# Performance work log

Hardware: AMD Instinct MI355X
Metric: run time of the kernel (lower is better)

The kernel has to match this reference:

```python
import jax, jax.numpy as jnp
import numpy as np

EMBED_DIM = 512
NUM_HEADS = 8
HEAD_DIM = EMBED_DIM // NUM_HEADS
EDGE_HIDDEN = 512
B, L = 2, 512


def setup_inputs() -> dict:
    key = jax.random.key(0)
    ks = jax.random.split(key, 16)
    s = 0.02
    inp = {
        "query": jax.random.normal(ks[0], (B, L, EMBED_DIM), jnp.float32),
        "key_in": jax.random.normal(ks[1], (B, L, EMBED_DIM), jnp.float32),
        "value": jax.random.normal(ks[2], (B, L, EMBED_DIM), jnp.float32),
        "edge_representation": jax.random.normal(ks[3], (B, L, L), jnp.float32),
        # projection weights stored as [in, out]: y = x @ W + b
        "Wq": jax.random.normal(ks[4], (EMBED_DIM, EMBED_DIM), jnp.float32) * s,
        "bq": jnp.zeros((EMBED_DIM,), jnp.float32),
        "Wk": jax.random.normal(ks[5], (EMBED_DIM, EMBED_DIM), jnp.float32) * s,
        "bk": jnp.zeros((EMBED_DIM,), jnp.float32),
        "Wv": jax.random.normal(ks[6], (EMBED_DIM, EMBED_DIM), jnp.float32) * s,
        "bv": jnp.zeros((EMBED_DIM,), jnp.float32),
        "Wo": jax.random.normal(ks[7], (EMBED_DIM, EMBED_DIM), jnp.float32) * s,
        "bo": jnp.zeros((EMBED_DIM,), jnp.float32),
        # edge MLP: Linear(1 -> 512) -> ReLU -> Linear(512 -> num_heads)
        "We1": jax.random.normal(ks[8], (1, EDGE_HIDDEN), jnp.float32) * s,
        "be1": jnp.zeros((EDGE_HIDDEN,), jnp.float32),
        "We2": jax.random.normal(ks[9], (EDGE_HIDDEN, NUM_HEADS), jnp.float32) * s,
        "be2": jnp.zeros((NUM_HEADS,), jnp.float32),
    }
    return inp


def reference(query, key_in, value, edge_representation,
              Wq, bq, Wk, bk, Wv, bv, Wo, bo, We1, be1, We2, be2):
    Bc, Lc, _ = query.shape
    # project and split heads: [B, H, L, Dh]
    def split_heads(x):
        return x.reshape(Bc, Lc, NUM_HEADS, HEAD_DIM).transpose(0, 2, 1, 3)
    Q = split_heads(query @ Wq + bq)
    K = split_heads(key_in @ Wk + bk)
    V = split_heads(value @ Wv + bv)
    # edge MLP on scalar edge features: [B, L, L, 1] -> [B, L, L, H]
    e = edge_representation[..., None]
    h = jax.nn.relu(e * We1[0] + be1)          # [B, L, L, 512]
    edge_bias = h @ We2 + be2                   # [B, L, L, H]
    scale = 1.0 / jnp.sqrt(jnp.asarray(HEAD_DIM, query.dtype))
    scores = jnp.einsum("bhqd,bhkd->bhqk", Q, K) * scale
    scores = scores + edge_bias.transpose(0, 3, 1, 2)  # [B, H, L, L]
    attn = jax.nn.softmax(scores, axis=-1)
    out = jnp.einsum("bhqk,bhkd->bhqd", attn, V)
    out = out.transpose(0, 2, 1, 3).reshape(Bc, Lc, EMBED_DIM)
    return out @ Wo + bo
```

## Files before the change

### kernel.cpp

```cpp
#include <hip/hip_runtime.h>
#include <hip/hip_bf16.h>

typedef __attribute__((ext_vector_type(8))) short bf16x8;
typedef __attribute__((ext_vector_type(4))) float f32x4;

#define LOG2E 1.44269504088896340736f

#define QB_OFF 2621440
#define KB_OFF 3145728
#define VT_OFF 3670016
#define AO_OFF 4194304
#define T_B   9437184
#define A_B   (T_B + 4096)
#define C_B   (A_B + 20480)

struct MegaArgs {
  const float *xq, *xk, *xv, *eg;
  const float *wq, *wk, *wv, *wo;
  const float *bq, *bk, *bv, *bo;
  const float *w1, *b1, *we2, *be2;
  float* out;
  unsigned short* wsb;
  float *wsT, *wsA, *wsC;
};

__device__ __forceinline__ unsigned short f2bf(float f) {
  union { __hip_bfloat16 h; unsigned short u; } c;
  c.h = __float2bfloat16(f);
  return c.u;
}

__device__ __forceinline__ uint4 pack8(float4 a, float4 b) {
  union { unsigned short us[8]; uint4 u; } r;
  r.us[0] = f2bf(a.x); r.us[1] = f2bf(a.y); r.us[2] = f2bf(a.z); r.us[3] = f2bf(a.w);
  r.us[4] = f2bf(b.x); r.us[5] = f2bf(b.y); r.us[6] = f2bf(b.z); r.us[7] = f2bf(b.w);
  return r.u;
}

__device__ __forceinline__ bf16x8 pack8v(float4 a, float4 b) {
  union { uint4 u; bf16x8 v; } r;
  r.u = pack8(a, b);
  return r.v;
}

__device__ void prep_block(const MegaArgs& a, char* smem) {
  float* sT   = (float*)smem;
  int*   sIdx = (int*)(smem + 2048);
  float (*sDA)[8] = (float (*)[8])(smem + 4096);
  float (*sDC)[8] = (float (*)[8])(smem + 20480);
  float* sA0 = (float*)(smem + 36864);
  float* sC0 = (float*)(smem + 36896);
  int tid = threadIdx.x, lane = tid & 63, w = tid >> 6;
  float accA[8] = {0,0,0,0,0,0,0,0}, accC[8] = {0,0,0,0,0,0,0,0};
  for (int e = 0; e < 2; ++e) {
    int p = tid + e * 256;
    float ww = a.w1[p], bb = a.b1[p];
    sT[p] = (ww != 0.f) ? (-bb / ww) : -3.4e38f;
    sIdx[p] = p;
#pragma unroll
    for (int h = 0; h < 8; ++h) {
      float w2 = a.we2[p * 8 + h];
      if (ww < 0.f)       { accA[h] += w2 * ww; accC[h] += w2 * bb; }
      else if (ww == 0.f) { accC[h] += w2 * fmaxf(bb, 0.f); }
    }
  }
  __syncthreads();
  for (int size = 2; size <= 512; size <<= 1) {
    for (int stride = size >> 1; stride > 0; stride >>= 1) {
      if (size >= 256 && stride >= 64) __syncthreads();
      else __builtin_amdgcn_wave_barrier();
      int p = tid;
      int i = ((p / stride) * (stride << 1)) + (p % stride);
      int j = i + stride;
      bool up = ((i & size) == 0);
      float ti = sT[i], tj = sT[j];
      if (up ? (ti > tj) : (ti < tj)) {
        sT[i] = tj; sT[j] = ti;
        int t = sIdx[i]; sIdx[i] = sIdx[j]; sIdx[j] = t;
      }
    }
  }
  for (int off = 32; off > 0; off >>= 1) {
#pragma unroll
    for (int h = 0; h < 8; ++h) {
      accA[h] += __shfl_xor(accA[h], off);
      accC[h] += __shfl_xor(accC[h], off);
    }
  }
  if (lane == 0) {
#pragma unroll
    for (int h = 0; h < 8; ++h) { sDA[w][h] = accA[h]; sDC[w][h] = accC[h]; }
  }
  __syncthreads();
  if (tid < 8) {
    sA0[tid] = sDA[0][tid] + sDA[1][tid] + sDA[2][tid] + sDA[3][tid];
    sC0[tid] = sDC[0][tid] + sDC[1][tid] + sDC[2][tid] + sDC[3][tid] + a.be2[tid];
  }
  __syncthreads();
  for (int e = 0; e < 2; ++e) {
    int p = tid + e * 256;
    int k = sIdx[p];
    float wk = a.w1[k], bk2 = a.b1[k];
#pragma unroll
    for (int h = 0; h < 8; ++h) {
      float w2 = a.we2[k * 8 + h];
      float da = 0.f, dc = 0.f;
      if (wk > 0.f)      { da =  w2 * wk; dc =  w2 * bk2; }
      else if (wk < 0.f) { da = -w2 * wk; dc = -w2 * bk2; }
      sDA[p][h] = da; sDC[p][h] = dc;
    }
  }
  __syncthreads();
  for (int off = 1; off < 512; off <<= 1) {
    float ra[2][8], rc[2][8];
#pragma unroll
    for (int e = 0; e < 2; ++e) {
      int p = tid + e * 256;
      if (p >= off) {
#pragma unroll
        for (int h = 0; h < 8; ++h) { ra[e][h] = sDA[p - off][h]; rc[e][h] = sDC[p - off][h]; }
      }
    }
    __syncthreads();
#pragma unroll
    for (int e = 0; e < 2; ++e) {
      int p = tid + e * 256;
      if (p >= off) {
#pragma unroll
        for (int h = 0; h < 8; ++h) { sDA[p][h] += ra[e][h]; sDC[p][h] += rc[e][h]; }
      }
    }
    __syncthreads();
  }
  bool n0 = (tid == 0) || (sT[tid] != sT[tid - 1]);
  bool n1 = (sT[tid + 256] != sT[tid + 255]);
  unsigned long long m0 = __ballot(n0), m1 = __ballot(n1);
  unsigned long long below = (1ull << lane) - 1ull;
  int loc0 = __popcll(m0 & below), loc1 = __popcll(m1 & below);
  int* tot = sIdx;
  if (lane == 0) { tot[w] = __popcll(m0); tot[4 + w] = __popcll(m1); }
  __syncthreads();
  int t[8];
#pragma unroll
  for (int j = 0; j < 8; ++j) t[j] = tot[j];
  int nuniq = t[0] + t[1] + t[2] + t[3] + t[4] + t[5] + t[6] + t[7];
  int off0 = 0, off1 = t[0] + t[1] + t[2] + t[3];
  for (int j = 0; j < 4; ++j) {
    if (j < w) { off0 += t[j]; off1 += t[4 + j]; }
  }
  if (n0) {
    int u = off0 + loc0;
    a.wsT[u] = sT[tid];
    if (tid == 0) {
#pragma unroll
      for (int h = 0; h < 8; ++h) { a.wsA[h * 513] = sA0[h]; a.wsC[h * 513] = sC0[h]; }
    } else {
#pragma unroll
      for (int h = 0; h < 8; ++h) {
        a.wsA[h * 513 + u] = sA0[h] + sDA[tid - 1][h];
        a.wsC[h * 513 + u] = sC0[h] + sDC[tid - 1][h];
      }
    }
  }
  if (n1) {
    int u = off1 + loc1;
    a.wsT[u] = sT[tid + 256];
#pragma unroll
    for (int h = 0; h < 8; ++h) {
      a.wsA[h * 513 + u] = sA0[h] + sDA[tid + 255][h];
      a.wsC[h * 513 + u] = sC0[h] + sDC[tid + 255][h];
    }
  }
  if (tid == 0) {
#pragma unroll
    for (int h = 0; h < 8; ++h) {
      a.wsA[h * 513 + nuniq] = sA0[h] + sDA[511][h];
      a.wsC[h * 513 + nuniq] = sC0[h] + sDC[511][h];
    }
    *(int*)(a.wsT + 512) = nuniq;
  }
}

__device__ void gemm_fast(const float* __restrict__ Af, const unsigned short* __restrict__ Ab,
                          const float* __restrict__ W, const float* __restrict__ bias,
                          void* out, int mode, int m0, int n0, char* smem) {
  int tid = threadIdx.x, wave = tid >> 6, lane = tid & 63;
  int quad = lane >> 4, l16 = lane & 15;
  int lr = tid >> 2, ls = tid & 3;
  int kb8 = lr >> 3, klo = lr & 7;
  int slot = ((kb8 ^ ls) << 3) + klo;
#pragma unroll
  for (int c = 0; c < 8; ++c) {
    unsigned short (*sBt)[72] = (unsigned short (*)[72])(smem + c * 9216);
    const float4* wp = (const float4*)(W + (size_t)(c * 64 + lr) * 512 + n0 + ls * 16);
    float4 w0 = wp[0], w1 = wp[1], w2 = wp[2], w3 = wp[3];
    int nb = ls * 16;
    sBt[nb + 0][slot] = f2bf(w0.x);  sBt[nb + 1][slot] = f2bf(w0.y);
    sBt[nb + 2][slot] = f2bf(w0.z);  sBt[nb + 3][slot] = f2bf(w0.w);
    sBt[nb + 4][slot] = f2bf(w1.x);  sBt[nb + 5][slot] = f2bf(w1.y);
    sBt[nb + 6][slot] = f2bf(w1.z);  sBt[nb + 7][slot] = f2bf(w1.w);
    sBt[nb + 8][slot] = f2bf(w2.x);  sBt[nb + 9][slot] = f2bf(w2.y);
    sBt[nb + 10][slot] = f2bf(w2.z); sBt[nb + 11][slot] = f2bf(w2.w);
    sBt[nb + 12][slot] = f2bf(w3.x); sBt[nb + 13][slot] = f2bf(w3.y);
    sBt[nb + 14][slot] = f2bf(w3.z); sBt[nb + 15][slot] = f2bf(w3.w);
  }
  __syncthreads();
  f32x4 acc[4] = {{0.f,0.f,0.f,0.f},{0.f,0.f,0.f,0.f},{0.f,0.f,0.f,0.f},{0.f,0.f,0.f,0.f}};
  const float*          arf = Af ? Af + (size_t)(m0 + wave * 16 + l16) * 512 : nullptr;
  const unsigned short* arb = Ab ? Ab + (size_t)(m0 + wave * 16 + l16) * 512 : nullptr;
#pragma unroll
  for (int kf = 0; kf < 16; ++kf) {
    bf16x8 af;
    if (Af) {
      const float4* ap = (const float4*)(arf + kf * 32 + quad * 8);
      af = pack8v(ap[0], ap[1]);
    } else {
      af = *(const bf16x8*)(arb + kf * 32 + quad * 8);
    }
    unsigned short (*sBt)[72] = (unsigned short (*)[72])(smem + (kf >> 1) * 9216);
    int g = (kf & 1) * 4 + quad;
#pragma unroll
    for (int nt = 0; nt < 4; ++nt) {
      bf16x8 bf = *(const bf16x8*)&sBt[nt * 16 + l16][(g ^ nt) * 8];
      acc[nt] = __builtin_amdgcn_mfma_f32_16x16x32_bf16(af, bf, acc[nt], 0, 0, 0);
    }
  }
  int mbase = m0 + wave * 16 + quad * 4;
#pragma unroll
  for (int nt = 0; nt < 4; ++nt) {
    int n = n0 + nt * 16 + l16;
    float bv = bias[n];
#pragma unroll
    for (int r = 0; r < 4; ++r) {
      float v = acc[nt][r] + bv;
      int m = mbase + r;
      if (mode == 0) {
        int b = m >> 9, l = m & 511, hh = n >> 6, d = n & 63;
        ((unsigned short*)out)[(((size_t)(b * 8 + hh) * 512) + l) * 64 + d] = f2bf(v);
      } else if (mode == 1) {
        ((float*)out)[(size_t)m * 512 + n] = v;
      } else {
        int b = m >> 9, l = m & 511, hh = n >> 6, d = n & 63;
        ((unsigned short*)out)[(((size_t)(b * 8 + hh) * 64) + d) * 512 + l] = f2bf(v);
      }
    }
  }
}

__device__ void attn_block(const MegaArgs& a, int qt, int h, int b, char* smem) {
  float* sT  = (float*)smem;
  float* sAh = (float*)(smem + 2048);
  float* sCh = (float*)(smem + 4112);
  unsigned short (*sP)[16][136] = (unsigned short (*)[16][136])(smem + 6176);
  float (*sO)[4][16][16] = (float (*)[4][16][16])(smem + 23584);
  float (*sM)[16] = (float (*)[16])(smem + 39968);
  float (*sL)[16] = (float (*)[16])(smem + 40224);
  const unsigned short* Qb = a.wsb + QB_OFF;
  const unsigned short* Kb = a.wsb + KB_OFF;
  const unsigned short* Vt = a.wsb + VT_OFF;
  int bh = b * 8 + h;
  int q0 = qt * 16;
  int tid = threadIdx.x, wave = tid >> 6, lane = tid & 63;
  int quad = lane >> 4, l16 = lane & 15;
  int nu = *(const int*)(a.wsT + 512);
  for (int i = tid; i < nu; i += 256) sT[i] = a.wsT[i];
  for (int i = tid; i <= nu; i += 256) { sAh[i] = a.wsA[h * 513 + i]; sCh[i] = a.wsC[h * 513 + i]; }
  int key_base = wave * 128;
  float egv[4][2][4];
#pragma unroll
  for (int kt = 0; kt < 4; ++kt)
#pragma unroll
    for (int half = 0; half < 2; ++half)
#pragma unroll
      for (int r = 0; r < 4; ++r) {
        int eidx = (b * 512 + q0 + quad * 4 + r) * 512 + key_base + kt * 32 + half * 16 + l16;
        egv[kt][half][r] = a.eg[eidx];
      }
  const unsigned short* qp = Qb + ((size_t)bh * 512 + q0 + l16) * 64 + quad * 8;
  bf16x8 qf0 = *(const bf16x8*)qp;
  bf16x8 qf1 = *(const bf16x8*)(qp + 32);
  bf16x8 kfr[4][2][2];
#pragma unroll
  for (int kt = 0; kt < 4; ++kt)
#pragma unroll
    for (int half = 0; half < 2; ++half) {
      const unsigned short* kp =
          Kb + ((size_t)bh * 512 + key_base + kt * 32 + half * 16 + l16) * 64 + quad * 8;
      kfr[kt][half][0] = *(const bf16x8*)kp;
      kfr[kt][half][1] = *(const bf16x8*)(kp + 32);
    }
  f32x4 S[4][2];
#pragma unroll
  for (int kt = 0; kt < 4; ++kt)
#pragma unroll
    for (int half = 0; half < 2; ++half) {
      f32x4 acc = {0.f, 0.f, 0.f, 0.f};
      acc = __builtin_amdgcn_mfma_f32_16x16x32_bf16(qf0, kfr[kt][half][0], acc, 0, 0, 0);
      acc = __builtin_amdgcn_mfma_f32_16x16x32_bf16(qf1, kfr[kt][half][1], acc, 0, 0, 0);
      S[kt][half] = acc;
    }
  __syncthreads();
#pragma unroll
  for (int kt = 0; kt < 4; ++kt)
#pragma unroll
    for (int half = 0; half < 2; ++half)
#pragma unroll
      for (int r = 0; r < 4; ++r) {
        float ev = egv[kt][half][r];
        int lo = 0, hi = nu;
        while (lo < hi) {
          int mid = (lo + hi) >> 1;
          bool c = sT[mid] < ev;
          lo = c ? mid + 1 : lo;
          hi = c ? hi : mid;
        }
        S[kt][half][r] = S[kt][half][r] * 0.125f + sAh[lo] * ev + sCh[lo];
      }
  bf16x8 vfr[4][4];
#pragma unroll
  for (int kt = 0; kt < 4; ++kt)
#pragma unroll
    for (int nt = 0; nt < 4; ++nt)
      vfr[kt][nt] = *(const bf16x8*)(Vt + ((size_t)bh * 64 + nt * 16 + l16) * 512 +
                                     key_base + kt * 32 + quad * 8);
  float m_w[4], l_w[4];
#pragma unroll
  for (int r = 0; r < 4; ++r) {
    float mx = -3.4e38f;
#pragma unroll
    for (int kt = 0; kt < 4; ++kt) { mx = fmaxf(mx, fmaxf(S[kt][0][r], S[kt][1][r])); }
    for (int off = 1; off < 16; off <<= 1) mx = fmaxf(mx, __shfl_xor(mx, off, 64));
    float s = 0.f;
#pragma unroll
    for (int kt = 0; kt < 4; ++kt)
#pragma unroll
      for (int half = 0; half < 2; ++half) {
        float p = exp2f((S[kt][half][r] - mx) * LOG2E);
        S[kt][half][r] = p; s += p;
      }
    for (int off = 1; off < 16; off <<= 1) s += __shfl_xor(s, off, 64);
    m_w[r] = mx; l_w[r] = s;
  }
#pragma unroll
  for (int kt = 0; kt < 4; ++kt)
#pragma unroll
    for (int half = 0; half < 2; ++half)
#pragma unroll
      for (int r = 0; r < 4; ++r)
        sP[wave][quad * 4 + r][kt * 32 + half * 16 + l16] = f2bf(S[kt][half][r]);
  __builtin_amdgcn_wave_barrier();
  f32x4 Oacc[4] = {{0.f,0.f,0.f,0.f},{0.f,0.f,0.f,0.f},{0.f,0.f,0.f,0.f},{0.f,0.f,0.f,0.f}};
#pragma unroll
  for (int kt = 0; kt < 4; ++kt) {
    bf16x8 pf = *(const bf16x8*)&sP[wave][l16][kt * 32 + quad * 8];
#pragma unroll
    for (int nt = 0; nt < 4; ++nt)
      Oacc[nt] = __builtin_amdgcn_mfma_f32_16x16x32_bf16(pf, vfr[kt][nt], Oacc[nt], 0, 0, 0);
  }
  if (l16 == 0) {
#pragma unroll
    for (int r = 0; r < 4; ++r) { sM[wave][quad * 4 + r] = m_w[r]; sL[wave][quad * 4 + r] = l_w[r]; }
  }
#pragma unroll
  for (int nt = 0; nt < 4; ++nt)
#pragma unroll
    for (int r = 0; r < 4; ++r)
      sO[wave][nt][quad * 4 + r][l16] = Oacc[nt][r];
  __syncthreads();
#pragma unroll
  for (int r = 0; r < 4; ++r) {
    int row = quad * 4 + r;
    float M = fmaxf(fmaxf(sM[0][row], sM[1][row]), fmaxf(sM[2][row], sM[3][row]));
    float L = 0.f, Ov = 0.f;
#pragma unroll
    for (int wv = 0; wv < 4; ++wv) {
      float f = exp2f((sM[wv][row] - M) * LOG2E);
      L += f * sL[wv][row];
      Ov += f * sO[wv][wave][row][l16];
    }
    float v = Ov / L;
    (a.wsb + AO_OFF)[((size_t)(b * 512 + q0 + row)) * 512 + h * 64 + wave * 16 + l16] = f2bf(v);
  }
}

__global__ __launch_bounds__(256, 2) void k1(MegaArgs a) {
  __shared__ __align__(16) char smem[73728];
  int blk = blockIdx.x;
  if (blk == 0) {
    prep_block(a, smem);
  } else {
    int g = blk - 1, z = g >> 7, rem = g & 127;
    const float* A    = (z == 0) ? a.xq : (z == 1) ? a.xk : a.xv;
    const float* W    = (z == 0) ? a.wq : (z == 1) ? a.wk : a.wv;
    const float* bias = (z == 0) ? a.bq : (z == 1) ? a.bk : a.bv;
    void* outp = (void*)(a.wsb + ((z == 0) ? QB_OFF : (z == 1) ? KB_OFF : VT_OFF));
    gemm_fast(A, nullptr, W, bias, outp, (z == 2) ? 2 : 0, (rem & 15) * 64, (rem >> 4) * 64, smem);
  }
}

__global__ __launch_bounds__(256, 2) void k2(MegaArgs a) {
  __shared__ __align__(16) char smem[40480];
  int blk = blockIdx.x;
  attn_block(a, blk & 31, (blk >> 5) & 7, blk >> 8, smem);
}

__global__ __launch_bounds__(256, 2) void k3(MegaArgs a) {
  __shared__ __align__(16) char smem[73728];
  gemm_fast(nullptr, a.wsb + AO_OFF, a.wo, a.bo, (void*)a.out, 1,
            (blockIdx.x & 15) * 64, (blockIdx.x >> 4) * 64, smem);
}

extern "C" void kernel_launch(void* const* d_in, const int* in_sizes, int n_in,
                              void* d_out, int out_size, void* d_ws, size_t ws_size,
                              hipStream_t stream) {
  MegaArgs a;
  a.xq  = (const float*)d_in[0];
  a.xk  = (const float*)d_in[1];
  a.xv  = (const float*)d_in[2];
  a.eg  = (const float*)d_in[3];
  a.wq  = (const float*)d_in[4];
  a.bq  = (const float*)d_in[5];
  a.wk  = (const float*)d_in[6];
  a.bk  = (const float*)d_in[7];
  a.wv  = (const float*)d_in[8];
  a.bv  = (const float*)d_in[9];
  a.wo  = (const float*)d_in[10];
  a.bo  = (const float*)d_in[11];
  a.w1  = (const float*)d_in[12];
  a.b1  = (const float*)d_in[13];
  a.we2 = (const float*)d_in[14];
  a.be2 = (const float*)d_in[15];
  a.out = (float*)d_out;
  a.wsb = (unsigned short*)d_ws;
  a.wsT = (float*)((char*)d_ws + T_B);
  a.wsA = (float*)((char*)d_ws + A_B);
  a.wsC = (float*)((char*)d_ws + C_B);

  k1<<<385, 256, 0, stream>>>(a);
  k2<<<512, 256, 0, stream>>>(a);
  k3<<<128, 256, 0, stream>>>(a);
}
```

Measured before the change: 134.9 us.

## Fuse three kernels into one persistent kernel with global atomic barriers

Merges the projection, attention and output-projection kernels into a single 512-block launch separated by software grid barriers built on agent-scope atomics, with a memset resetting the counters each call. The edge-MLP prep block signals readiness through a separate flag, so attention blocks can run their QK^T MFMAs before waiting on it. K and V fragments are now loaded next to their MFMAs instead of being preloaded into register arrays. The aim is to remove kernel launch gaps and hide the prep latency. In exchange it depends on all 512 blocks being co-resident, since the grid barrier deadlocks otherwise, and it adds spin-wait and memset overhead.

```diff
diff --git a/kernel.cpp b/kernel.cpp
--- a/kernel.cpp
+++ b/kernel.cpp
@@ -13,6 +13,8 @@
 #define T_B   9437184
 #define A_B   (T_B + 4096)
 #define C_B   (A_B + 20480)
+#define BAR_B 16777216
+#define NBLK  512
 
 struct MegaArgs {
   const float *xq, *xk, *xv, *eg;
@@ -41,6 +43,20 @@
   union { uint4 u; bf16x8 v; } r;
   r.u = pack8(a, b);
   return r.v;
+}
+
+__device__ __forceinline__ void gbar(unsigned int* cnt, unsigned int target, int arrive) {
+  __syncthreads();
+  if (threadIdx.x == 0) {
+    __threadfence();
+    if (arrive)
+      __hip_atomic_fetch_add(cnt, 1u, __ATOMIC_RELEASE, __HIP_MEMORY_SCOPE_AGENT);
+    while (__hip_atomic_load(cnt, __ATOMIC_ACQUIRE, __HIP_MEMORY_SCOPE_AGENT) < target) {
+      __builtin_amdgcn_s_sleep(8);
+    }
+    __threadfence();
+  }
+  __syncthreads();
 }
 
 __device__ void prep_block(const MegaArgs& a, char* smem) {
@@ -247,7 +263,8 @@
   }
 }
 
-__device__ void attn_block(const MegaArgs& a, int qt, int h, int b, char* smem) {
+__device__ void attn_block6(const MegaArgs& a, int qt, int h, int b, char* smem,
+                            unsigned int* flag) {
   float* sT  = (float*)smem;
   float* sAh = (float*)(smem + 2048);
   float* sCh = (float*)(smem + 4112);
@@ -262,43 +279,45 @@
   int q0 = qt * 16;
   int tid = threadIdx.x, wave = tid >> 6, lane = tid & 63;
   int quad = lane >> 4, l16 = lane & 15;
+  int key_base = wave * 128;
+  float egv[4][2][4];
+#pragma unroll
+  for (int kt = 0; kt < 4; ++kt)
+#pragma unroll
+    for (int half = 0; half < 2; ++half)
+#pragma unroll
+      for (int r = 0; r < 4; ++r) {
+        int eidx = (b * 512 + q0 + quad * 4 + r) * 512 + key_base + kt * 32 + half * 16 + l16;
+        egv[kt][half][r] = a.eg[eidx];
+      }
+  const unsigned short* qp = Qb + ((size_t)bh * 512 + q0 + l16) * 64 + quad * 8;
+  bf16x8 qf0 = *(const bf16x8*)qp;
+  bf16x8 qf1 = *(const bf16x8*)(qp + 32);
+  f32x4 S[4][2];
+#pragma unroll
+  for (int kt = 0; kt < 4; ++kt) {
+    int key0 = key_base + kt * 32;
+#pragma unroll
+    for (int half = 0; half < 2; ++half) {
+      const unsigned short* kp = Kb + ((size_t)bh * 512 + key0 + half * 16 + l16) * 64 + quad * 8;
+      bf16x8 kf0 = *(const bf16x8*)kp;
+      bf16x8 kf1 = *(const bf16x8*)(kp + 32);
+      f32x4 acc = {0.f, 0.f, 0.f, 0.f};
+      acc = __builtin_amdgcn_mfma_f32_16x16x32_bf16(qf0, kf0, acc, 0, 0, 0);
+      acc = __builtin_amdgcn_mfma_f32_16x16x32_bf16(qf1, kf1, acc, 0, 0, 0);
+      S[kt][half] = acc;
+    }
+  }
+  if (tid == 0) {
+    while (__hip_atomic_load(flag, __ATOMIC_ACQUIRE, __HIP_MEMORY_SCOPE_AGENT) == 0u) {
+      __builtin_amdgcn_s_sleep(8);
+    }
+    __threadfence();
+  }
+  __syncthreads();
   int nu = *(const int*)(a.wsT + 512);
   for (int i = tid; i < nu; i += 256) sT[i] = a.wsT[i];
   for (int i = tid; i <= nu; i += 256) { sAh[i] = a.wsA[h * 513 + i]; sCh[i] = a.wsC[h * 513 + i]; }
-  int key_base = wave * 128;
-  float egv[4][2][4];
-#pragma unroll
-  for (int kt = 0; kt < 4; ++kt)
-#pragma unroll
-    for (int half = 0; half < 2; ++half)
-#pragma unroll
-      for (int r = 0; r < 4; ++r) {
-        int eidx = (b * 512 + q0 + quad * 4 + r) * 512 + key_base + kt * 32 + half * 16 + l16;
-        egv[kt][half][r] = a.eg[eidx];
-      }
-  const unsigned short* qp = Qb + ((size_t)bh * 512 + q0 + l16) * 64 + quad * 8;
-  bf16x8 qf0 = *(const bf16x8*)qp;
-  bf16x8 qf1 = *(const bf16x8*)(qp + 32);
-  bf16x8 kfr[4][2][2];
-#pragma unroll
-  for (int kt = 0; kt < 4; ++kt)
-#pragma unroll
-    for (int half = 0; half < 2; ++half) {
-      const unsigned short* kp =
-          Kb + ((size_t)bh * 512 + key_base + kt * 32 + half * 16 + l16) * 64 + quad * 8;
-      kfr[kt][half][0] = *(const bf16x8*)kp;
-      kfr[kt][half][1] = *(const bf16x8*)(kp + 32);
-    }
-  f32x4 S[4][2];
-#pragma unroll
-  for (int kt = 0; kt < 4; ++kt)
-#pragma unroll
-    for (int half = 0; half < 2; ++half) {
-      f32x4 acc = {0.f, 0.f, 0.f, 0.f};
-      acc = __builtin_amdgcn_mfma_f32_16x16x32_bf16(qf0, kfr[kt][half][0], acc, 0, 0, 0);
-      acc = __builtin_amdgcn_mfma_f32_16x16x32_bf16(qf1, kfr[kt][half][1], acc, 0, 0, 0);
-      S[kt][half] = acc;
-    }
   __syncthreads();
 #pragma unroll
   for (int kt = 0; kt < 4; ++kt)
@@ -316,13 +335,6 @@
         }
         S[kt][half][r] = S[kt][half][r] * 0.125f + sAh[lo] * ev + sCh[lo];
       }
-  bf16x8 vfr[4][4];
-#pragma unroll
-  for (int kt = 0; kt < 4; ++kt)
-#pragma unroll
-    for (int nt = 0; nt < 4; ++nt)
-      vfr[kt][nt] = *(const bf16x8*)(Vt + ((size_t)bh * 64 + nt * 16 + l16) * 512 +
-                                     key_base + kt * 32 + quad * 8);
   float m_w[4], l_w[4];
 #pragma unroll
   for (int r = 0; r < 4; ++r) {
@@ -352,10 +364,13 @@
   f32x4 Oacc[4] = {{0.f,0.f,0.f,0.f},{0.f,0.f,0.f,0.f},{0.f,0.f,0.f,0.f},{0.f,0.f,0.f,0.f}};
 #pragma unroll
   for (int kt = 0; kt < 4; ++kt) {
+    int key0 = key_base + kt * 32;
     bf16x8 pf = *(const bf16x8*)&sP[wave][l16][kt * 32 + quad * 8];
 #pragma unroll
-    for (int nt = 0; nt < 4; ++nt)
-      Oacc[nt] = __builtin_amdgcn_mfma_f32_16x16x32_bf16(pf, vfr[kt][nt], Oacc[nt], 0, 0, 0);
+    for (int nt = 0; nt < 4; ++nt) {
+      bf16x8 vf = *(const bf16x8*)(Vt + ((size_t)bh * 64 + nt * 16 + l16) * 512 + key0 + quad * 8);
+      Oacc[nt] = __builtin_amdgcn_mfma_f32_16x16x32_bf16(pf, vf, Oacc[nt], 0, 0, 0);
+    }
   }
   if (l16 == 0) {
 #pragma unroll
@@ -383,31 +398,42 @@
   }
 }
 
-__global__ __launch_bounds__(256, 2) void k1(MegaArgs a) {
+__global__ __launch_bounds__(256, 2) void kfused(MegaArgs a) {
   __shared__ __align__(16) char smem[73728];
+  unsigned int* bar0 = (unsigned int*)((char*)a.wsb + BAR_B);
+  unsigned int* flag = bar0 + 16;
+  unsigned int* bar1 = bar0 + 32;
   int blk = blockIdx.x;
+
   if (blk == 0) {
     prep_block(a, smem);
+    __syncthreads();
+    if (threadIdx.x == 0) {
+      __threadfence();
+      __hip_atomic_store(flag, 1u, __ATOMIC_RELEASE, __HIP_MEMORY_SCOPE_AGENT);
+    }
+    gbar(bar0, NBLK - 1, 0);
   } else {
-    int g = blk - 1, z = g >> 7, rem = g & 127;
-    const float* A    = (z == 0) ? a.xq : (z == 1) ? a.xk : a.xv;
-    const float* W    = (z == 0) ? a.wq : (z == 1) ? a.wk : a.wv;
-    const float* bias = (z == 0) ? a.bq : (z == 1) ? a.bk : a.bv;
-    void* outp = (void*)(a.wsb + ((z == 0) ? QB_OFF : (z == 1) ? KB_OFF : VT_OFF));
-    gemm_fast(A, nullptr, W, bias, outp, (z == 2) ? 2 : 0, (rem & 15) * 64, (rem >> 4) * 64, smem);
-  }
-}
-
-__global__ __launch_bounds__(256, 2) void k2(MegaArgs a) {
-  __shared__ __align__(16) char smem[40480];
-  int blk = blockIdx.x;
-  attn_block(a, blk & 31, (blk >> 5) & 7, blk >> 8, smem);
-}
-
-__global__ __launch_bounds__(256, 2) void k3(MegaArgs a) {
-  __shared__ __align__(16) char smem[73728];
-  gemm_fast(nullptr, a.wsb + AO_OFF, a.wo, a.bo, (void*)a.out, 1,
-            (blockIdx.x & 15) * 64, (blockIdx.x >> 4) * 64, smem);
+    if (blk <= 384) {
+      int g = blk - 1, z = g >> 7, rem = g & 127;
+      const float* A    = (z == 0) ? a.xq : (z == 1) ? a.xk : a.xv;
+      const float* W    = (z == 0) ? a.wq : (z == 1) ? a.wk : a.wv;
+      const float* bias = (z == 0) ? a.bq : (z == 1) ? a.bk : a.bv;
+      void* outp = (void*)(a.wsb + ((z == 0) ? QB_OFF : (z == 1) ? KB_OFF : VT_OFF));
+      gemm_fast(A, nullptr, W, bias, outp, (z == 2) ? 2 : 0,
+                (rem & 15) * 64, (rem >> 4) * 64, smem);
+    }
+    gbar(bar0, NBLK - 1, 1);
+  }
+
+  attn_block6(a, blk & 31, (blk >> 5) & 7, blk >> 8, smem, flag);
+
+  gbar(bar1, NBLK, 1);
+
+  if (blk < 128) {
+    gemm_fast(nullptr, a.wsb + AO_OFF, a.wo, a.bo, (void*)a.out, 1,
+              (blk & 15) * 64, (blk >> 4) * 64, smem);
+  }
 }
 
 extern "C" void kernel_launch(void* const* d_in, const int* in_sizes, int n_in,
@@ -436,7 +462,6 @@
   a.wsA = (float*)((char*)d_ws + A_B);
   a.wsC = (float*)((char*)d_ws + C_B);
 
-  k1<<<385, 256, 0, stream>>>(a);
-  k2<<<512, 256, 0, stream>>>(a);
-  k3<<<128, 256, 0, stream>>>(a);
-}
+  hipMemsetAsync((char*)d_ws + BAR_B, 0, 256, stream);
+  kfused<<<NBLK, 256, 0, stream>>>(a);
+}
```

Result: slower. 329.7 us (+144.4%).
